# Performance work log

Hardware: AMD Instinct MI355X
Metric: run time of the kernel (lower is better)

The kernel has to match this reference:

```python
import jax, jax.numpy as jnp
import numpy as np

REG = 0.1  # sinkhorn_reg from __init__


def setup_inputs() -> dict:
    key = jax.random.key(0)
    ks = jax.random.split(key, 13)
    B, T, C, H, W = 16, 128, 256, 32, 32  # batch, num_tokens, hidden c, mask HxW
    HW = H * W
    s = 0.02
    return {
        "F_a": jax.random.normal(ks[0], (B, T, C), jnp.float32),
        "F_s": jax.random.normal(ks[1], (B, HW, C), jnp.float32),
        "M_s": jax.random.randint(ks[2], (B, H, W), 0, 2, jnp.int32),
        # learned params (torch Linear: y = x @ W + b, W stored here as [in, out])
        "W_aQ": jax.random.normal(ks[3], (C, HW), jnp.float32) * s,
        "b_aQ": jnp.zeros((HW,), jnp.float32),
        "W_sK": jax.random.normal(ks[4], (C, HW), jnp.float32) * s,
        "b_sK": jnp.zeros((HW,), jnp.float32),
        "W_sV": jax.random.normal(ks[5], (C, C), jnp.float32) * s,
        "b_sV": jnp.zeros((C,), jnp.float32),
        "W1": jax.random.normal(ks[6], (C, 3 * C), jnp.float32) * s,
        "b1": jnp.zeros((3 * C,), jnp.float32),
        "W2": jax.random.normal(ks[7], (3 * C, C), jnp.float32) * s,
        "b2": jnp.zeros((C,), jnp.float32),
        "max_iter_ot": 100,
    }


def reference(F_a, F_s, M_s, W_aQ, b_aQ, W_sK, b_sK, W_sV, b_sV, W1, b1, W2, b2, max_iter_ot):
    B, T, _ = F_a.shape
    m = M_s.reshape(B, -1).astype(jnp.float32)              # [B, HW] binary fg mask
    neg = jnp.where(m[:, None, :] == 1.0, 0.0, -jnp.inf)    # additive attention mask

    # Attention_Eqn3: S = softmax(Q_a K_s^T / 1 + M)
    Q = F_a @ W_aQ + b_aQ                                   # [B, T, HW]
    K_s = F_s @ W_sK + b_sK                                 # [B, HW, HW]
    QK = jnp.einsum("bth,bkh->btk", Q, K_s)                 # [B, T, HW]
    S = jax.nn.softmax(QK + neg, axis=2)                    # masked cols -> 0

    # Vectorized masked Sinkhorn OT across the batch.
    # Zero target marginal on masked columns is equivalent to POT's sinkhorn
    # on the foreground-only cost matrix (their v stays 0, zeroing those cols).
    cost = 1.0 - S
    Kmat = jnp.exp(-cost / REG)                             # [B, T, HW], strictly > 0
    num_fg = jnp.sum(m, axis=1, keepdims=True)              # [B, 1]
    bvec = m / num_fg                                       # [B, HW] uniform over fg
    avec = jnp.full((B, T), 1.0 / T, jnp.float32)

    u0 = jnp.full((B, T), 1.0 / T, jnp.float32)
    v0 = jnp.zeros_like(bvec)

    def step(carry, _):
        u, _v = carry
        Ktu = jnp.einsum("bth,bt->bh", Kmat, u)
        v = jnp.where(bvec > 0, bvec / Ktu, 0.0)
        Kv = jnp.einsum("bth,bh->bt", Kmat, v)
        u = avec / Kv
        return (u, v), None

    (u, v), _ = jax.lax.scan(step, (u0, v0), None, length=max_iter_ot)
    S_hat = u[:, :, None] * Kmat * v[:, None, :]            # [B, T, HW]

    # Attention_Eqn7: FFN(S_hat @ V_s); dropout is identity in eval mode
    V_s = F_s @ W_sV + b_sV                                 # [B, HW, C]
    out = jnp.einsum("btk,bkc->btc", S_hat, V_s)            # [B, T, C]
    h = jax.nn.relu(out @ W1 + b1)
    return h @ W2 + b2
```

## Files before the change

### kernel.cpp

```cpp
#include <hip/hip_runtime.h>
#include <cstdint>

#define T_DIM 128
#define C_DIM 256
#define HW_DIM 1024
#define B_DIM 16
#define NJR 8
#define PARTC 640
#define CHK 10
#define TOL 2e-6f
#define LDP 72

typedef __bf16 bf16x8 __attribute__((ext_vector_type(8)));
typedef float f32x4 __attribute__((ext_vector_type(4)));

__device__ __forceinline__ float fast_rcp(float x) {
  return __builtin_amdgcn_rcpf(x);
}

__device__ __forceinline__ unsigned short f2bf(float x) {
  unsigned u = __float_as_uint(x);
  u += 0x7fffu + ((u >> 16) & 1u);
  return (unsigned short)(u >> 16);
}
__device__ __forceinline__ float bf2f(unsigned short h) {
  return __uint_as_float((unsigned)h << 16);
}

__global__ __launch_bounds__(256) void prep_kernel(const int* __restrict__ Ms,
                                                   int* __restrict__ nfg,
                                                   int* __restrict__ pos)
{
  const int b = blockIdx.x, tid = threadIdx.x;
  const int4 m4 = *(const int4*)(Ms + b * HW_DIM + tid * 4);
  const int c = m4.x + m4.y + m4.z + m4.w;
  const int lane = tid & 63, w = tid >> 6;
  int pre = c;
  #pragma unroll
  for (int o = 1; o < 64; o <<= 1) { int t = __shfl_up(pre, (unsigned)o); if (lane >= o) pre += t; }
  __shared__ int wtot[4];
  if (lane == 63) wtot[w] = pre;
  __syncthreads();
  int base = 0;
  #pragma unroll
  for (int i = 0; i < 4; i++) if (i < w) base += wtot[i];
  const int excl = base + pre - c;
  if (tid == 0) nfg[b] = wtot[0] + wtot[1] + wtot[2] + wtot[3];
  int p = excl;
  const int mm[4] = {m4.x, m4.y, m4.z, m4.w};
  #pragma unroll
  for (int q = 0; q < 4; q++) {
    pos[b * HW_DIM + tid * 4 + q] = mm[q] ? p : -1;
    p += mm[q];
  }
}

__global__ __launch_bounds__(256) void wvec_kernel(
    const float* __restrict__ W_aQ, const float* __restrict__ b_aQ,
    const float* __restrict__ W_sK, const float* __restrict__ b_sK,
    float* __restrict__ w0, float* __restrict__ wq, float* __restrict__ s0)
{
  const int wid = blockIdx.x * 4 + (threadIdx.x >> 6);
  const int lane = threadIdx.x & 63;
  if (wid > 512) return;
  float acc = 0.f;
  if (wid < 256) {
    #pragma unroll 4
    for (int j = 0; j < 16; j++) { int h = lane + 64 * j; acc = fmaf(b_aQ[h], W_sK[(size_t)wid * 1024 + h], acc); }
  } else if (wid < 512) {
    const int c = wid - 256;
    #pragma unroll 4
    for (int j = 0; j < 16; j++) { int h = lane + 64 * j; acc = fmaf(W_aQ[(size_t)c * 1024 + h], b_sK[h], acc); }
  } else {
    #pragma unroll 4
    for (int j = 0; j < 16; j++) { int h = lane + 64 * j; acc = fmaf(b_aQ[h], b_sK[h], acc); }
  }
  #pragma unroll
  for (int o = 32; o; o >>= 1) acc += __shfl_xor(acc, o);
  if (lane == 0) {
    if (wid < 256) w0[wid] = acc;
    else if (wid < 512) wq[wid - 256] = acc;
    else s0[0] = acc;
  }
}

__global__ __launch_bounds__(256) void qb_kernel(const float* __restrict__ F_a,
    const float* __restrict__ wq, const float* __restrict__ s0, float* __restrict__ qb)
{
  const int r = blockIdx.x * 4 + (threadIdx.x >> 6);
  const int lane = threadIdx.x & 63;
  float acc = 0.f;
  #pragma unroll
  for (int j = 0; j < 4; j++) { int c = lane + 64 * j; acc = fmaf(F_a[(size_t)r * 256 + c], wq[c], acc); }
  #pragma unroll
  for (int o = 32; o; o >>= 1) acc += __shfl_xor(acc, o);
  if (lane == 0) qb[r] = acc + s0[0];
}

__global__ __launch_bounds__(256) void split_kernel(const float* __restrict__ S,
    unsigned short* __restrict__ Dh, unsigned short* __restrict__ Dl, int n8)
{
  const int i = blockIdx.x * 256 + threadIdx.x;
  if (i >= n8) return;
  const float4 x0 = ((const float4*)S)[2 * i];
  const float4 x1 = ((const float4*)S)[2 * i + 1];
  const float xs[8] = {x0.x, x0.y, x0.z, x0.w, x1.x, x1.y, x1.z, x1.w};
  unsigned hs[8], ls[8];
  #pragma unroll
  for (int q = 0; q < 8; q++) {
    const unsigned short h = f2bf(xs[q]);
    hs[q] = h;
    ls[q] = f2bf(xs[q] - bf2f(h));
  }
  uint4 oh, ol;
  oh.x = hs[0] | (hs[1] << 16); oh.y = hs[2] | (hs[3] << 16);
  oh.z = hs[4] | (hs[5] << 16); oh.w = hs[6] | (hs[7] << 16);
  ol.x = ls[0] | (ls[1] << 16); ol.y = ls[2] | (ls[3] << 16);
  ol.z = ls[4] | (ls[5] << 16); ol.w = ls[6] | (ls[7] << 16);
  ((uint4*)Dh)[i] = oh;
  ((uint4*)Dl)[i] = ol;
}

__global__ __launch_bounds__(256) void splitT_kernel(const float* __restrict__ S, int R, int C,
    long long sS, unsigned short* __restrict__ Dh, unsigned short* __restrict__ Dl, long long sD)
{
  __shared__ float t[32][33];
  const int bz = blockIdx.z;
  S += sS * bz;  Dh += sD * bz;  Dl += sD * bz;
  const int c0 = blockIdx.x * 32, r0 = blockIdx.y * 32;
  const int tx = threadIdx.x & 31, ty = threadIdx.x >> 5;
  #pragma unroll
  for (int i = 0; i < 4; i++) t[ty + 8 * i][tx] = S[(size_t)(r0 + ty + 8 * i) * C + c0 + tx];
  __syncthreads();
  #pragma unroll
  for (int i = 0; i < 4; i++) {
    const int c = ty + 8 * i;
    const float x = t[tx][c];
    const unsigned short h = f2bf(x);
    Dh[(size_t)(c0 + c) * R + r0 + tx] = h;
    Dl[(size_t)(c0 + c) * R + r0 + tx] = f2bf(x - bf2f(h));
  }
}

template<int BIAS, bool RELU, int OUTM>
__global__ __launch_bounds__(256) void mgemm_kernel(
    const unsigned short* __restrict__ Ah, const unsigned short* __restrict__ Al, int lda, long long sA,
    const unsigned short* __restrict__ Bh, const unsigned short* __restrict__ Bl, int ldb, long long sB,
    void* __restrict__ C0, void* __restrict__ C1, int ldc, long long sC,
    int K, const float* __restrict__ bias, int sBias, float bscale)
{
  __shared__ __align__(16) unsigned short AsH[64 * LDP];
  __shared__ __align__(16) unsigned short AsL[64 * LDP];
  __shared__ __align__(16) unsigned short BsH[64 * LDP];
  __shared__ __align__(16) unsigned short BsL[64 * LDP];
  const int bz = blockIdx.z;
  Ah += sA * bz;  Al += sA * bz;  Bh += sB * bz;  Bl += sB * bz;
  const int m0 = blockIdx.y * 64, n0 = blockIdx.x * 64;
  const int tid = threadIdx.x;
  const int lr = tid >> 2, lc = (tid & 3) * 16;
  const int w = tid >> 6, lane = tid & 63;
  const int wm = (w >> 1) * 32, wn = (w & 1) * 32;
  const int fr = lane & 15, fk = (lane >> 4) * 8;
  const f32x4 zz = {0.f, 0.f, 0.f, 0.f};
  f32x4 acc[2][2] = {{zz, zz}, {zz, zz}};
  const size_t abase = (size_t)(m0 + lr) * lda + lc;
  const size_t bbase = (size_t)(n0 + lr) * ldb + lc;
  uint4 ah0 = *(const uint4*)(Ah + abase), ah1 = *(const uint4*)(Ah + abase + 8);
  uint4 al0 = *(const uint4*)(Al + abase), al1 = *(const uint4*)(Al + abase + 8);
  uint4 bh0 = *(const uint4*)(Bh + bbase), bh1 = *(const uint4*)(Bh + bbase + 8);
  uint4 bl0 = *(const uint4*)(Bl + bbase), bl1 = *(const uint4*)(Bl + bbase + 8);
  const int NT = K >> 6;
  for (int t = 0; t < NT; ++t) {
    __syncthreads();
    *(uint4*)&AsH[lr * LDP + lc] = ah0;  *(uint4*)&AsH[lr * LDP + lc + 8] = ah1;
    *(uint4*)&AsL[lr * LDP + lc] = al0;  *(uint4*)&AsL[lr * LDP + lc + 8] = al1;
    *(uint4*)&BsH[lr * LDP + lc] = bh0;  *(uint4*)&BsH[lr * LDP + lc + 8] = bh1;
    *(uint4*)&BsL[lr * LDP + lc] = bl0;  *(uint4*)&BsL[lr * LDP + lc + 8] = bl1;
    __syncthreads();
    if (t + 1 < NT) {
      const size_t ka = abase + (size_t)(t + 1) * 64;
      const size_t kb = bbase + (size_t)(t + 1) * 64;
      ah0 = *(const uint4*)(Ah + ka);  ah1 = *(const uint4*)(Ah + ka + 8);
      al0 = *(const uint4*)(Al + ka);  al1 = *(const uint4*)(Al + ka + 8);
      bh0 = *(const uint4*)(Bh + kb);  bh1 = *(const uint4*)(Bh + kb + 8);
      bl0 = *(const uint4*)(Bl + kb);  bl1 = *(const uint4*)(Bl + kb + 8);
    }
    #pragma unroll
    for (int ks = 0; ks < 2; ++ks) {
      const bf16x8 aH0 = *(const bf16x8*)&AsH[(wm + fr) * LDP + ks * 32 + fk];
      const bf16x8 aH1 = *(const bf16x8*)&AsH[(wm + 16 + fr) * LDP + ks * 32 + fk];
      const bf16x8 aL0 = *(const bf16x8*)&AsL[(wm + fr) * LDP + ks * 32 + fk];
      const bf16x8 aL1 = *(const bf16x8*)&AsL[(wm + 16 + fr) * LDP + ks * 32 + fk];
      const bf16x8 bH0 = *(const bf16x8*)&BsH[(wn + fr) * LDP + ks * 32 + fk];
      const bf16x8 bH1 = *(const bf16x8*)&BsH[(wn + 16 + fr) * LDP + ks * 32 + fk];
      const bf16x8 bL0 = *(const bf16x8*)&BsL[(wn + fr) * LDP + ks * 32 + fk];
      const bf16x8 bL1 = *(const bf16x8*)&BsL[(wn + 16 + fr) * LDP + ks * 32 + fk];
      acc[0][0] = __builtin_amdgcn_mfma_f32_16x16x32_bf16(aH0, bH0, acc[0][0], 0, 0, 0);
      acc[0][1] = __builtin_amdgcn_mfma_f32_16x16x32_bf16(aH0, bH1, acc[0][1], 0, 0, 0);
      acc[1][0] = __builtin_amdgcn_mfma_f32_16x16x32_bf16(aH1, bH0, acc[1][0], 0, 0, 0);
      acc[1][1] = __builtin_amdgcn_mfma_f32_16x16x32_bf16(aH1, bH1, acc[1][1], 0, 0, 0);
      acc[0][0] = __builtin_amdgcn_mfma_f32_16x16x32_bf16(aH0, bL0, acc[0][0], 0, 0, 0);
      acc[0][1] = __builtin_amdgcn_mfma_f32_16x16x32_bf16(aH0, bL1, acc[0][1], 0, 0, 0);
      acc[1][0] = __builtin_amdgcn_mfma_f32_16x16x32_bf16(aH1, bL0, acc[1][0], 0, 0, 0);
      acc[1][1] = __builtin_amdgcn_mfma_f32_16x16x32_bf16(aH1, bL1, acc[1][1], 0, 0, 0);
      acc[0][0] = __builtin_amdgcn_mfma_f32_16x16x32_bf16(aL0, bH0, acc[0][0], 0, 0, 0);
      acc[0][1] = __builtin_amdgcn_mfma_f32_16x16x32_bf16(aL0, bH1, acc[0][1], 0, 0, 0);
      acc[1][0] = __builtin_amdgcn_mfma_f32_16x16x32_bf16(aL1, bH0, acc[1][0], 0, 0, 0);
      acc[1][1] = __builtin_amdgcn_mfma_f32_16x16x32_bf16(aL1, bH1, acc[1][1], 0, 0, 0);
    }
  }
  const long long cb = sC * bz;
  #pragma unroll
  for (int fi = 0; fi < 2; ++fi) {
    #pragma unroll
    for (int r = 0; r < 4; ++r) {
      const int m = m0 + wm + fi * 16 + (lane >> 4) * 4 + r;
      float rb = 0.f;
      if (BIAS == 2) rb = bias[(size_t)sBias * bz + m];
      #pragma unroll
      for (int fj = 0; fj < 2; ++fj) {
        const int n = n0 + wn + fj * 16 + fr;
        float val = acc[fi][fj][r];
        if (BIAS == 1) val += bscale * bias[n];
        if (BIAS == 2) val += rb;
        if (RELU) val = fmaxf(val, 0.f);
        if (OUTM == 0) {
          ((float*)C0)[cb + (size_t)m * ldc + n] = val;
        } else {
          const unsigned short h = f2bf(val);
          ((unsigned short*)C0)[cb + (size_t)m * ldc + n] = h;
          ((unsigned short*)C1)[cb + (size_t)m * ldc + n] = f2bf(val - bf2f(h));
        }
      }
    }
  }
}

__global__ __launch_bounds__(256) void softmax_kernel(
    const float* __restrict__ QK, const int* __restrict__ Ms,
    const int* __restrict__ pos, float* __restrict__ Kc)
{
  const int r = blockIdx.x;
  const int b = r >> 7;
  const int tid = threadIdx.x;
  const float4 x = *(const float4*)(QK + (size_t)r * HW_DIM + tid * 4);
  const int4 m4 = *(const int4*)(Ms + b * HW_DIM + tid * 4);
  float mx = -3.0e38f;
  if (m4.x) mx = x.x;
  if (m4.y) mx = fmaxf(mx, x.y);
  if (m4.z) mx = fmaxf(mx, x.z);
  if (m4.w) mx = fmaxf(mx, x.w);
  #pragma unroll
  for (int o = 32; o; o >>= 1) mx = fmaxf(mx, __shfl_xor(mx, o));
  __shared__ float red[4];
  const int lane = tid & 63, w = tid >> 6;
  if (lane == 0) red[w] = mx;
  __syncthreads();
  const float gmax = fmaxf(fmaxf(red[0], red[1]), fmaxf(red[2], red[3]));
  __syncthreads();
  const float e0 = m4.x ? __expf(x.x - gmax) : 0.f;
  const float e1 = m4.y ? __expf(x.y - gmax) : 0.f;
  const float e2 = m4.z ? __expf(x.z - gmax) : 0.f;
  const float e3 = m4.w ? __expf(x.w - gmax) : 0.f;
  float s = e0 + e1 + e2 + e3;
  #pragma unroll
  for (int o = 32; o; o >>= 1) s += __shfl_xor(s, o);
  if (lane == 0) red[w] = s;
  __syncthreads();
  const float inv = 1.0f / (red[0] + red[1] + red[2] + red[3]);
  const int4 p4 = *(const int4*)(pos + b * HW_DIM + tid * 4);
  const float ev[4] = {e0, e1, e2, e3};
  const int pp[4] = {p4.x, p4.y, p4.z, p4.w};
  #pragma unroll
  for (int q = 0; q < 4; q++)
    if (pp[q] >= 0) Kc[(size_t)r * HW_DIM + pp[q]] = __expf(fmaf(10.f, ev[q] * inv, -10.f));
}

__global__ __launch_bounds__(1024, 4) void sinkhorn_kernel(
    const float* __restrict__ Kc, const int* __restrict__ nfg_arr,
    const int* __restrict__ pos, const int* __restrict__ maxIter,
    float* __restrict__ u_out, float* __restrict__ v_out)
{
  const int b = blockIdx.x;
  const int tid = threadIdx.x;
  const int tg = tid >> 6, kg = tid & 63;
  const int nfg = nfg_arr[b];
  const float inv_nfg = 1.0f / (float)nfg;
  const int niter = *maxIter;
  const int njall = (nfg + 63) >> 6;
  __shared__ float part[16][PARTC];
  __shared__ float v_s[HW_DIM];
  __shared__ float u_s[T_DIM];
  __shared__ int conv;
  const float* KB = Kc + (size_t)(b * T_DIM) * HW_DIM;

  if (njall * 64 <= PARTC) {
    const int njr = (njall < NJR) ? njall : NJR;
    float kreg[8][NJR];
    #pragma unroll
    for (int j = 0; j < NJR; j++) {
      #pragma unroll
      for (int i = 0; i < 8; i++) {
        const int col = kg + 64 * j;
        float vle = 0.f;
        if (j < njr && col < nfg) vle = KB[(size_t)(tg * 8 + i) * HW_DIM + col];
        kreg[i][j] = vle;
      }
    }
    if (tid < T_DIM) u_s[tid] = 1.0f / 128.0f;
    if (tid == 0) conv = 1;
    const float bv = (tid < nfg) ? inv_nfg : 0.f;
    float u_prev = 1.0f / 128.0f;
    __syncthreads();

    for (int it = 0; it < niter; ++it) {
      float uu[8];
      #pragma unroll
      for (int i = 0; i < 8; i++) uu[i] = u_s[tg * 8 + i];
      #pragma unroll
      for (int j = 0; j < NJR; j++) {
        if (j < njr) {
          float s = 0.f;
          #pragma unroll
          for (int i = 0; i < 8; i++) s = fmaf(kreg[i][j], uu[i], s);
          part[tg][kg + 64 * j] = s;
        }
      }
      for (int j = NJR; j < njall; ++j) {
        const int col = kg + 64 * j;
        float s = 0.f;
        #pragma unroll
        for (int i = 0; i < 8; i++) {
          const float kk = (col < nfg) ? KB[(size_t)(tg * 8 + i) * HW_DIM + col] : 0.f;
          s = fmaf(kk, uu[i], s);
        }
        part[tg][col] = s;
      }
      __syncthreads();
      if (it != 0 && (it % CHK) == 0) {
        if (conv) break;
      }
      const int checknow = ((it % CHK) == (CHK - 1));
      if (checknow && tid == 0) conv = 1;
      {
        float vv = 0.f;
        if (tid < nfg) {
          float s = 0.f;
          #pragma unroll
          for (int g = 0; g < 16; g++) s += part[g][tid];
          vv = bv * fast_rcp(s);
        }
        v_s[tid] = vv;
      }
      __syncthreads();
      float vload[NJR];
      #pragma unroll
      for (int j = 0; j < NJR; j++) vload[j] = (j < njr) ? v_s[kg + 64 * j] : 0.f;
      float kv[8];
      #pragma unroll
      for (int i = 0; i < 8; i++) {
        float s = 0.f;
        #pragma unroll
        for (int j = 0; j < NJR; j++) s = fmaf(kreg[i][j], vload[j], s);
        kv[i] = s;
      }
      for (int j = NJR; j < njall; ++j) {
        const int col = kg + 64 * j;
        const float vv = v_s[col];
        #pragma unroll
        for (int i = 0; i < 8; i++) {
          const float kk = (col < nfg) ? KB[(size_t)(tg * 8 + i) * HW_DIM + col] : 0.f;
          kv[i] = fmaf(kk, vv, kv[i]);
        }
      }
      float k2[4];
      #pragma unroll
      for (int p = 0; p < 4; p++) {
        const float g = (kg & 1) ? kv[2 * p] : kv[2 * p + 1];
        const float r = __shfl_xor(g, 1);
        k2[p] = ((kg & 1) ? kv[2 * p + 1] : kv[2 * p]) + r;
      }
      float k3[2];
      #pragma unroll
      for (int q = 0; q < 2; q++) {
        const float g = (kg & 2) ? k2[2 * q] : k2[2 * q + 1];
        const float r = __shfl_xor(g, 2);
        k3[q] = ((kg & 2) ? k2[2 * q + 1] : k2[2 * q]) + r;
      }
      float t;
      {
        const float g = (kg & 4) ? k3[0] : k3[1];
        const float r = __shfl_xor(g, 4);
        t = ((kg & 4) ? k3[1] : k3[0]) + r;
      }
      t += __shfl_xor(t, 8);
      t += __shfl_xor(t, 16);
      t += __shfl_xor(t, 32);
      const float u_new = 0.0078125f * fast_rcp(t);
      if (kg < 8) u_s[tg * 8 + kg] = u_new;
      if (checknow) {
        const int ok = (fabsf(u_new - u_prev) <= TOL * fabsf(u_new));
        if (!__all(ok) && kg == 0) conv = 0;
      }
      u_prev = u_new;
    }
    __syncthreads();
    if (tid < T_DIM) u_out[b * T_DIM + tid] = u_s[tid];
    {
      const int p = pos[b * HW_DIM + tid];
      v_out[b * HW_DIM + tid] = (p >= 0) ? v_s[p] : 0.f;
    }
  } else {
    if (tid < T_DIM) u_s[tid] = 1.0f / 128.0f;
    const float bv = (tid < nfg) ? inv_nfg : 0.f;
    __syncthreads();
    for (int it = 0; it < niter; ++it) {
      float vv = 0.f;
      if (tid < nfg) {
        float s = 0.f;
        for (int t = 0; t < T_DIM; t++) s = fmaf(KB[(size_t)t * HW_DIM + tid], u_s[t], s);
        vv = bv * fast_rcp(s);
      }
      v_s[tid] = vv;
      __syncthreads();
      #pragma unroll
      for (int r8 = 0; r8 < 8; r8++) {
        const int r = tg * 8 + r8;
        float s = 0.f;
        for (int j = 0; j < 16; j++) {
          const int col = kg + 64 * j;
          if (col < nfg) s = fmaf(KB[(size_t)r * HW_DIM + col], v_s[col], s);
        }
        #pragma unroll
        for (int o = 32; o; o >>= 1) s += __shfl_xor(s, o);
        if (kg == 0) u_s[r] = 0.0078125f * fast_rcp(s);
      }
      __syncthreads();
    }
    if (tid < T_DIM) u_out[b * T_DIM + tid] = u_s[tid];
    const int p = pos[b * HW_DIM + tid];
    v_out[b * HW_DIM + tid] = (p >= 0) ? v_s[p] : 0.f;
  }
}

__global__ __launch_bounds__(256) void shat_kernel(const float* __restrict__ Kc,
    const int* __restrict__ pos, const float* __restrict__ u, const float* __restrict__ v,
    unsigned short* __restrict__ ShH, unsigned short* __restrict__ ShL)
{
  const int r = blockIdx.x, b = r >> 7, tid = threadIdx.x;
  const float uu = u[r];
  const int4 p4 = *(const int4*)(pos + b * HW_DIM + tid * 4);
  const float4 vv = *(const float4*)(v + (size_t)b * HW_DIM + tid * 4);
  const float* kr = Kc + (size_t)r * HW_DIM;
  const float ov[4] = {
    (p4.x >= 0) ? uu * kr[p4.x] * vv.x : 0.f,
    (p4.y >= 0) ? uu * kr[p4.y] * vv.y : 0.f,
    (p4.z >= 0) ? uu * kr[p4.z] * vv.z : 0.f,
    (p4.w >= 0) ? uu * kr[p4.w] * vv.w : 0.f };
  unsigned hs[4], ls[4];
  #pragma unroll
  for (int q = 0; q < 4; q++) {
    const unsigned short h = f2bf(ov[q]);
    hs[q] = h;  ls[q] = f2bf(ov[q] - bf2f(h));
  }
  uint2 ph, pl;
  ph.x = hs[0] | (hs[1] << 16);  ph.y = hs[2] | (hs[3] << 16);
  pl.x = ls[0] | (ls[1] << 16);  pl.y = ls[2] | (ls[3] << 16);
  *(uint2*)(ShH + (size_t)r * HW_DIM + tid * 4) = ph;
  *(uint2*)(ShL + (size_t)r * HW_DIM + tid * 4) = pl;
}

extern "C" void kernel_launch(void* const* d_in, const int* in_sizes, int n_in,
                              void* d_out, int out_size, void* d_ws, size_t ws_size,
                              hipStream_t stream)
{
  const float* F_a  = (const float*)d_in[0];
  const float* F_s  = (const float*)d_in[1];
  const int*   M_s  = (const int*)  d_in[2];
  const float* W_aQ = (const float*)d_in[3];
  const float* b_aQ = (const float*)d_in[4];
  const float* W_sK = (const float*)d_in[5];
  const float* b_sK = (const float*)d_in[6];
  const float* W_sV = (const float*)d_in[7];
  const float* b_sV = (const float*)d_in[8];
  const float* W1   = (const float*)d_in[9];
  const float* b1   = (const float*)d_in[10];
  const float* W2   = (const float*)d_in[11];
  const float* b2   = (const float*)d_in[12];
  const int* maxIter = (const int*)d_in[13];
  float* out = (float*)d_out;

  float* f = (float*)d_ws;
  float* w0 = f;  f += 256;
  float* wq = f;  f += 256;
  float* s0 = f;  f += 4;
  float* qb = f;  f += 2048;
  float* u  = f;  f += 2048;
  float* v  = f;  f += 16 * 1024;
  int* nfg  = (int*)f;  f += 16;
  int* pos  = (int*)f;  f += 16 * 1024;
  float* QK = f;  f += 2048 * 1024;
  float* Kc = f;  f += 2048 * 1024;
  unsigned short* us = (unsigned short*)f;
  #define ALLOC2(name, n) unsigned short* name##H = us; us += (n); unsigned short* name##L = us; us += (n);
  ALLOC2(F_a_,  2048 * 256)
  ALLOC2(W_sK_, 256 * 1024)
  ALLOC2(W_aQ_, 256 * 1024)
  ALLOC2(F_s_,  16 * 1024 * 256)
  ALLOC2(F_sT_, 16 * 256 * 1024)
  ALLOC2(MmT_,  256 * 256)
  ALLOC2(W_sVT_, 256 * 256)
  ALLOC2(W1T_, 768 * 256)
  ALLOC2(W2T_, 256 * 768)
  ALLOC2(P_,   2048 * 256)
  ALLOC2(Sh_,  2048 * 1024)
  ALLOC2(A2_,  2048 * 256)
  ALLOC2(o1_,  2048 * 256)
  ALLOC2(hh_,  2048 * 768)
  #undef ALLOC2

  prep_kernel<<<16, 256, 0, stream>>>(M_s, nfg, pos);
  wvec_kernel<<<129, 256, 0, stream>>>(W_aQ, b_aQ, W_sK, b_sK, w0, wq, s0);
  qb_kernel<<<512, 256, 0, stream>>>(F_a, wq, s0, qb);

  split_kernel<<<256, 256, 0, stream>>>(F_a, F_a_H, F_a_L, 2048 * 256 / 8);
  split_kernel<<<128, 256, 0, stream>>>(W_sK, W_sK_H, W_sK_L, 256 * 1024 / 8);
  split_kernel<<<128, 256, 0, stream>>>(W_aQ, W_aQ_H, W_aQ_L, 256 * 1024 / 8);
  split_kernel<<<2048, 256, 0, stream>>>(F_s, F_s_H, F_s_L, 16 * 1024 * 256 / 8);
  splitT_kernel<<<dim3(8, 8, 1),  256, 0, stream>>>(W_sV, 256, 256, 0, W_sVT_H, W_sVT_L, 0);
  splitT_kernel<<<dim3(24, 8, 1), 256, 0, stream>>>(W1, 256, 768, 0, W1T_H, W1T_L, 0);
  splitT_kernel<<<dim3(8, 24, 1), 256, 0, stream>>>(W2, 768, 256, 0, W2T_H, W2T_L, 0);
  splitT_kernel<<<dim3(8, 32, 16), 256, 0, stream>>>(F_s, 1024, 256, 1024 * 256, F_sT_H, F_sT_L, 256 * 1024);

  mgemm_kernel<0,false,1><<<dim3(4,4,1),256,0,stream>>>(
      W_sK_H, W_sK_L, 1024, 0, W_aQ_H, W_aQ_L, 1024, 0, MmT_H, MmT_L, 256, 0, 1024, nullptr, 0, 0.f);
  mgemm_kernel<1,false,1><<<dim3(4,32,1),256,0,stream>>>(
      F_a_H, F_a_L, 256, 0, MmT_H, MmT_L, 256, 0, P_H, P_L, 256, 0, 256, w0, 0, 1.0f);
  mgemm_kernel<2,false,0><<<dim3(16,2,16),256,0,stream>>>(
      P_H, P_L, 256, 128*256, F_s_H, F_s_L, 256, 1024*256, QK, nullptr, 1024, 128LL*1024, 256, qb, 128, 0.f);

  softmax_kernel<<<2048, 256, 0, stream>>>(QK, M_s, pos, Kc);
  sinkhorn_kernel<<<16, 1024, 0, stream>>>(Kc, nfg, pos, maxIter, u, v);
  shat_kernel<<<2048, 256, 0, stream>>>(Kc, pos, u, v, Sh_H, Sh_L);

  mgemm_kernel<0,false,1><<<dim3(4,2,16),256,0,stream>>>(
      Sh_H, Sh_L, 1024, 128*1024, F_sT_H, F_sT_L, 1024, 256*1024, A2_H, A2_L, 256, 128LL*256, 1024, nullptr, 0, 0.f);
  mgemm_kernel<1,false,1><<<dim3(4,32,1),256,0,stream>>>(
      A2_H, A2_L, 256, 0, W_sVT_H, W_sVT_L, 256, 0, o1_H, o1_L, 256, 0, 256, b_sV, 0, 0.0078125f);
  mgemm_kernel<1,true,1><<<dim3(12,32,1),256,0,stream>>>(
      o1_H, o1_L, 256, 0, W1T_H, W1T_L, 256, 0, hh_H, hh_L, 768, 0, 256, b1, 0, 1.0f);
  mgemm_kernel<1,false,0><<<dim3(4,32,1),256,0,stream>>>(
      hh_H, hh_L, 768, 0, W2T_H, W2T_L, 768, 0, out, nullptr, 256, 0, 768, b2, 0, 1.0f);
}
```

Before: 250.2 us.

## Fuse fp32-to-bf16 split and transpose into GEMM tile loads; merge setup kernels

Removes the separate split and splitT pre-pass kernels. The GEMMs now load raw fp32 operands and convert them in-register into hi/lo bf16 pairs while writing the shared-memory tile. For operands stored K-major, the transpose happens through scattered shared-memory stores. It also merges the prep and wvec kernels into one launch. This cuts about ten launches and the intermediate global traffic, but it re-converts each operand for every tile that reads it, and the transposed LDS stores may cause bank conflicts.

```diff
diff --git a/kernel.cpp b/kernel.cpp
--- a/kernel.cpp
+++ b/kernel.cpp
@@ -27,60 +27,58 @@
   return __uint_as_float((unsigned)h << 16);
 }
 
-__global__ __launch_bounds__(256) void prep_kernel(const int* __restrict__ Ms,
-                                                   int* __restrict__ nfg,
-                                                   int* __restrict__ pos)
-{
-  const int b = blockIdx.x, tid = threadIdx.x;
-  const int4 m4 = *(const int4*)(Ms + b * HW_DIM + tid * 4);
-  const int c = m4.x + m4.y + m4.z + m4.w;
-  const int lane = tid & 63, w = tid >> 6;
-  int pre = c;
-  #pragma unroll
-  for (int o = 1; o < 64; o <<= 1) { int t = __shfl_up(pre, (unsigned)o); if (lane >= o) pre += t; }
-  __shared__ int wtot[4];
-  if (lane == 63) wtot[w] = pre;
-  __syncthreads();
-  int base = 0;
-  #pragma unroll
-  for (int i = 0; i < 4; i++) if (i < w) base += wtot[i];
-  const int excl = base + pre - c;
-  if (tid == 0) nfg[b] = wtot[0] + wtot[1] + wtot[2] + wtot[3];
-  int p = excl;
-  const int mm[4] = {m4.x, m4.y, m4.z, m4.w};
-  #pragma unroll
-  for (int q = 0; q < 4; q++) {
-    pos[b * HW_DIM + tid * 4 + q] = mm[q] ? p : -1;
-    p += mm[q];
-  }
-}
-
-__global__ __launch_bounds__(256) void wvec_kernel(
+__global__ __launch_bounds__(256) void setup_kernel(const int* __restrict__ Ms,
+    int* __restrict__ nfg, int* __restrict__ pos,
     const float* __restrict__ W_aQ, const float* __restrict__ b_aQ,
     const float* __restrict__ W_sK, const float* __restrict__ b_sK,
     float* __restrict__ w0, float* __restrict__ wq, float* __restrict__ s0)
 {
-  const int wid = blockIdx.x * 4 + (threadIdx.x >> 6);
-  const int lane = threadIdx.x & 63;
-  if (wid > 512) return;
-  float acc = 0.f;
-  if (wid < 256) {
-    #pragma unroll 4
-    for (int j = 0; j < 16; j++) { int h = lane + 64 * j; acc = fmaf(b_aQ[h], W_sK[(size_t)wid * 1024 + h], acc); }
-  } else if (wid < 512) {
-    const int c = wid - 256;
-    #pragma unroll 4
-    for (int j = 0; j < 16; j++) { int h = lane + 64 * j; acc = fmaf(W_aQ[(size_t)c * 1024 + h], b_sK[h], acc); }
+  const int tid = threadIdx.x;
+  const int lane = tid & 63, w = tid >> 6;
+  if (blockIdx.x < 16) {
+    const int b = blockIdx.x;
+    const int4 m4 = *(const int4*)(Ms + b * HW_DIM + tid * 4);
+    const int c = m4.x + m4.y + m4.z + m4.w;
+    int pre = c;
+    #pragma unroll
+    for (int o = 1; o < 64; o <<= 1) { int t = __shfl_up(pre, (unsigned)o); if (lane >= o) pre += t; }
+    __shared__ int wtot[4];
+    if (lane == 63) wtot[w] = pre;
+    __syncthreads();
+    int base = 0;
+    #pragma unroll
+    for (int i = 0; i < 4; i++) if (i < w) base += wtot[i];
+    const int excl = base + pre - c;
+    if (tid == 0) nfg[b] = wtot[0] + wtot[1] + wtot[2] + wtot[3];
+    int p = excl;
+    const int mm[4] = {m4.x, m4.y, m4.z, m4.w};
+    #pragma unroll
+    for (int q = 0; q < 4; q++) {
+      pos[b * HW_DIM + tid * 4 + q] = mm[q] ? p : -1;
+      p += mm[q];
+    }
   } else {
-    #pragma unroll 4
-    for (int j = 0; j < 16; j++) { int h = lane + 64 * j; acc = fmaf(b_aQ[h], b_sK[h], acc); }
-  }
-  #pragma unroll
-  for (int o = 32; o; o >>= 1) acc += __shfl_xor(acc, o);
-  if (lane == 0) {
-    if (wid < 256) w0[wid] = acc;
-    else if (wid < 512) wq[wid - 256] = acc;
-    else s0[0] = acc;
+    const int wid = (blockIdx.x - 16) * 4 + w;
+    if (wid > 512) return;
+    float acc = 0.f;
+    if (wid < 256) {
+      #pragma unroll 4
+      for (int j = 0; j < 16; j++) { int h = lane + 64 * j; acc = fmaf(b_aQ[h], W_sK[(size_t)wid * 1024 + h], acc); }
+    } else if (wid < 512) {
+      const int c = wid - 256;
+      #pragma unroll 4
+      for (int j = 0; j < 16; j++) { int h = lane + 64 * j; acc = fmaf(W_aQ[(size_t)c * 1024 + h], b_sK[h], acc); }
+    } else {
+      #pragma unroll 4
+      for (int j = 0; j < 16; j++) { int h = lane + 64 * j; acc = fmaf(b_aQ[h], b_sK[h], acc); }
+    }
+    #pragma unroll
+    for (int o = 32; o; o >>= 1) acc += __shfl_xor(acc, o);
+    if (lane == 0) {
+      if (wid < 256) w0[wid] = acc;
+      else if (wid < 512) wq[wid - 256] = acc;
+      else s0[0] = acc;
+    }
   }
 }
 
@@ -97,55 +95,66 @@
   if (lane == 0) qb[r] = acc + s0[0];
 }
 
-__global__ __launch_bounds__(256) void split_kernel(const float* __restrict__ S,
-    unsigned short* __restrict__ Dh, unsigned short* __restrict__ Dl, int n8)
-{
-  const int i = blockIdx.x * 256 + threadIdx.x;
-  if (i >= n8) return;
-  const float4 x0 = ((const float4*)S)[2 * i];
-  const float4 x1 = ((const float4*)S)[2 * i + 1];
-  const float xs[8] = {x0.x, x0.y, x0.z, x0.w, x1.x, x1.y, x1.z, x1.w};
-  unsigned hs[8], ls[8];
-  #pragma unroll
-  for (int q = 0; q < 8; q++) {
-    const unsigned short h = f2bf(xs[q]);
-    hs[q] = h;
-    ls[q] = f2bf(xs[q] - bf2f(h));
-  }
-  uint4 oh, ol;
-  oh.x = hs[0] | (hs[1] << 16); oh.y = hs[2] | (hs[3] << 16);
-  oh.z = hs[4] | (hs[5] << 16); oh.w = hs[6] | (hs[7] << 16);
-  ol.x = ls[0] | (ls[1] << 16); ol.y = ls[2] | (ls[3] << 16);
-  ol.z = ls[4] | (ls[5] << 16); ol.w = ls[6] | (ls[7] << 16);
-  ((uint4*)Dh)[i] = oh;
-  ((uint4*)Dl)[i] = ol;
-}
-
-__global__ __launch_bounds__(256) void splitT_kernel(const float* __restrict__ S, int R, int C,
-    long long sS, unsigned short* __restrict__ Dh, unsigned short* __restrict__ Dl, long long sD)
-{
-  __shared__ float t[32][33];
-  const int bz = blockIdx.z;
-  S += sS * bz;  Dh += sD * bz;  Dl += sD * bz;
-  const int c0 = blockIdx.x * 32, r0 = blockIdx.y * 32;
-  const int tx = threadIdx.x & 31, ty = threadIdx.x >> 5;
-  #pragma unroll
-  for (int i = 0; i < 4; i++) t[ty + 8 * i][tx] = S[(size_t)(r0 + ty + 8 * i) * C + c0 + tx];
-  __syncthreads();
-  #pragma unroll
-  for (int i = 0; i < 4; i++) {
-    const int c = ty + 8 * i;
-    const float x = t[tx][c];
-    const unsigned short h = f2bf(x);
-    Dh[(size_t)(c0 + c) * R + r0 + tx] = h;
-    Dl[(size_t)(c0 + c) * R + r0 + tx] = f2bf(x - bf2f(h));
-  }
-}
-
-template<int BIAS, bool RELU, int OUTM>
+template<int MODE>
+__device__ __forceinline__ void ldG(uint4 r[4], const void* pH, const void* pL, size_t off) {
+  if constexpr (MODE == 2) {
+    const unsigned short* h = (const unsigned short*)pH + off;
+    const unsigned short* l = (const unsigned short*)pL + off;
+    r[0] = *(const uint4*)h;       r[1] = *(const uint4*)(h + 8);
+    r[2] = *(const uint4*)l;       r[3] = *(const uint4*)(l + 8);
+  } else {
+    const float* s = (const float*)pH + off;
+    r[0] = *(const uint4*)s;       r[1] = *(const uint4*)(s + 4);
+    r[2] = *(const uint4*)(s + 8); r[3] = *(const uint4*)(s + 12);
+  }
+}
+
+template<int MODE>
+__device__ __forceinline__ void stL(const uint4 r[4], unsigned short* __restrict__ H,
+                                    unsigned short* __restrict__ L, int lr, int lc) {
+  if constexpr (MODE == 2) {
+    *(uint4*)&H[lr * LDP + lc] = r[0];  *(uint4*)&H[lr * LDP + lc + 8] = r[1];
+    *(uint4*)&L[lr * LDP + lc] = r[2];  *(uint4*)&L[lr * LDP + lc + 8] = r[3];
+  } else {
+    float xs[16];
+    #pragma unroll
+    for (int q = 0; q < 4; q++) {
+      xs[4 * q + 0] = __uint_as_float(r[q].x);
+      xs[4 * q + 1] = __uint_as_float(r[q].y);
+      xs[4 * q + 2] = __uint_as_float(r[q].z);
+      xs[4 * q + 3] = __uint_as_float(r[q].w);
+    }
+    if constexpr (MODE == 0) {
+      unsigned hw[8], lw[8];
+      #pragma unroll
+      for (int e = 0; e < 8; e++) {
+        const unsigned short h0 = f2bf(xs[2 * e]), h1 = f2bf(xs[2 * e + 1]);
+        hw[e] = (unsigned)h0 | ((unsigned)h1 << 16);
+        const unsigned short l0 = f2bf(xs[2 * e] - bf2f(h0)), l1 = f2bf(xs[2 * e + 1] - bf2f(h1));
+        lw[e] = (unsigned)l0 | ((unsigned)l1 << 16);
+      }
+      uint4 a, b, c, d;
+      a.x = hw[0]; a.y = hw[1]; a.z = hw[2]; a.w = hw[3];
+      b.x = hw[4]; b.y = hw[5]; b.z = hw[6]; b.w = hw[7];
+      c.x = lw[0]; c.y = lw[1]; c.z = lw[2]; c.w = lw[3];
+      d.x = lw[4]; d.y = lw[5]; d.z = lw[6]; d.w = lw[7];
+      *(uint4*)&H[lr * LDP + lc] = a;  *(uint4*)&H[lr * LDP + lc + 8] = b;
+      *(uint4*)&L[lr * LDP + lc] = c;  *(uint4*)&L[lr * LDP + lc + 8] = d;
+    } else {
+      #pragma unroll
+      for (int e = 0; e < 16; e++) {
+        const unsigned short h = f2bf(xs[e]);
+        H[(lc + e) * LDP + lr] = h;
+        L[(lc + e) * LDP + lr] = f2bf(xs[e] - bf2f(h));
+      }
+    }
+  }
+}
+
+template<int AM, int BM, int BIAS, bool RELU, int OUTM>
 __global__ __launch_bounds__(256) void mgemm_kernel(
-    const unsigned short* __restrict__ Ah, const unsigned short* __restrict__ Al, int lda, long long sA,
-    const unsigned short* __restrict__ Bh, const unsigned short* __restrict__ Bl, int ldb, long long sB,
+    const void* __restrict__ Ah, const void* __restrict__ Al, int lda, long long sA,
+    const void* __restrict__ Bh, const void* __restrict__ Bl, int ldb, long long sB,
     void* __restrict__ C0, void* __restrict__ C1, int ldc, long long sC,
     int K, const float* __restrict__ bias, int sBias, float bscale)
 {
@@ -154,7 +163,11 @@
   __shared__ __align__(16) unsigned short BsH[64 * LDP];
   __shared__ __align__(16) unsigned short BsL[64 * LDP];
   const int bz = blockIdx.z;
-  Ah += sA * bz;  Al += sA * bz;  Bh += sB * bz;  Bl += sB * bz;
+  const void *Ab, *Alb, *Bb, *Blb;
+  if constexpr (AM == 2) { Ab = (const unsigned short*)Ah + sA * bz; Alb = (const unsigned short*)Al + sA * bz; }
+  else                   { Ab = (const float*)Ah + sA * bz;          Alb = nullptr; }
+  if constexpr (BM == 2) { Bb = (const unsigned short*)Bh + sB * bz; Blb = (const unsigned short*)Bl + sB * bz; }
+  else                   { Bb = (const float*)Bh + sB * bz;          Blb = nullptr; }
   const int m0 = blockIdx.y * 64, n0 = blockIdx.x * 64;
   const int tid = threadIdx.x;
   const int lr = tid >> 2, lc = (tid & 3) * 16;
@@ -163,27 +176,22 @@
   const int fr = lane & 15, fk = (lane >> 4) * 8;
   const f32x4 zz = {0.f, 0.f, 0.f, 0.f};
   f32x4 acc[2][2] = {{zz, zz}, {zz, zz}};
-  const size_t abase = (size_t)(m0 + lr) * lda + lc;
-  const size_t bbase = (size_t)(n0 + lr) * ldb + lc;
-  uint4 ah0 = *(const uint4*)(Ah + abase), ah1 = *(const uint4*)(Ah + abase + 8);
-  uint4 al0 = *(const uint4*)(Al + abase), al1 = *(const uint4*)(Al + abase + 8);
-  uint4 bh0 = *(const uint4*)(Bh + bbase), bh1 = *(const uint4*)(Bh + bbase + 8);
-  uint4 bl0 = *(const uint4*)(Bl + bbase), bl1 = *(const uint4*)(Bl + bbase + 8);
+  const size_t abase = (AM == 1) ? ((size_t)lr * lda + m0 + lc) : ((size_t)(m0 + lr) * lda + lc);
+  const size_t bbase = (BM == 1) ? ((size_t)lr * ldb + n0 + lc) : ((size_t)(n0 + lr) * ldb + lc);
+  const size_t astep = (AM == 1) ? (size_t)64 * lda : 64;
+  const size_t bstep = (BM == 1) ? (size_t)64 * ldb : 64;
+  uint4 ra[4], rb[4];
+  ldG<AM>(ra, Ab, Alb, abase);
+  ldG<BM>(rb, Bb, Blb, bbase);
   const int NT = K >> 6;
   for (int t = 0; t < NT; ++t) {
     __syncthreads();
-    *(uint4*)&AsH[lr * LDP + lc] = ah0;  *(uint4*)&AsH[lr * LDP + lc + 8] = ah1;
-    *(uint4*)&AsL[lr * LDP + lc] = al0;  *(uint4*)&AsL[lr * LDP + lc + 8] = al1;
-    *(uint4*)&BsH[lr * LDP + lc] = bh0;  *(uint4*)&BsH[lr * LDP + lc + 8] = bh1;
-    *(uint4*)&BsL[lr * LDP + lc] = bl0;  *(uint4*)&BsL[lr * LDP + lc + 8] = bl1;
+    stL<AM>(ra, AsH, AsL, lr, lc);
+    stL<BM>(rb, BsH, BsL, lr, lc);
     __syncthreads();
     if (t + 1 < NT) {
-      const size_t ka = abase + (size_t)(t + 1) * 64;
-      const size_t kb = bbase + (size_t)(t + 1) * 64;
-      ah0 = *(const uint4*)(Ah + ka);  ah1 = *(const uint4*)(Ah + ka + 8);
-      al0 = *(const uint4*)(Al + ka);  al1 = *(const uint4*)(Al + ka + 8);
-      bh0 = *(const uint4*)(Bh + kb);  bh1 = *(const uint4*)(Bh + kb + 8);
-      bl0 = *(const uint4*)(Bl + kb);  bl1 = *(const uint4*)(Bl + kb + 8);
+      ldG<AM>(ra, Ab, Alb, abase + (size_t)(t + 1) * astep);
+      ldG<BM>(rb, Bb, Blb, bbase + (size_t)(t + 1) * bstep);
     }
     #pragma unroll
     for (int ks = 0; ks < 2; ++ks) {
@@ -215,14 +223,14 @@
     #pragma unroll
     for (int r = 0; r < 4; ++r) {
       const int m = m0 + wm + fi * 16 + (lane >> 4) * 4 + r;
-      float rb = 0.f;
-      if (BIAS == 2) rb = bias[(size_t)sBias * bz + m];
+      float rb2 = 0.f;
+      if (BIAS == 2) rb2 = bias[(size_t)sBias * bz + m];
       #pragma unroll
       for (int fj = 0; fj < 2; ++fj) {
         const int n = n0 + wn + fj * 16 + fr;
         float val = acc[fi][fj][r];
         if (BIAS == 1) val += bscale * bias[n];
-        if (BIAS == 2) val += rb;
+        if (BIAS == 2) val += rb2;
         if (RELU) val = fmaxf(val, 0.f);
         if (OUTM == 0) {
           ((float*)C0)[cb + (size_t)m * ldc + n] = val;
@@ -503,15 +511,7 @@
   float* Kc = f;  f += 2048 * 1024;
   unsigned short* us = (unsigned short*)f;
   #define ALLOC2(name, n) unsigned short* name##H = us; us += (n); unsigned short* name##L = us; us += (n);
-  ALLOC2(F_a_,  2048 * 256)
-  ALLOC2(W_sK_, 256 * 1024)
-  ALLOC2(W_aQ_, 256 * 1024)
-  ALLOC2(F_s_,  16 * 1024 * 256)
-  ALLOC2(F_sT_, 16 * 256 * 1024)
-  ALLOC2(MmT_,  256 * 256)
-  ALLOC2(W_sVT_, 256 * 256)
-  ALLOC2(W1T_, 768 * 256)
-  ALLOC2(W2T_, 256 * 768)
+  ALLOC2(MmT_, 256 * 256)
   ALLOC2(P_,   2048 * 256)
   ALLOC2(Sh_,  2048 * 1024)
   ALLOC2(A2_,  2048 * 256)
@@ -519,36 +519,26 @@
   ALLOC2(hh_,  2048 * 768)
   #undef ALLOC2
 
-  prep_kernel<<<16, 256, 0, stream>>>(M_s, nfg, pos);
-  wvec_kernel<<<129, 256, 0, stream>>>(W_aQ, b_aQ, W_sK, b_sK, w0, wq, s0);
+  setup_kernel<<<145, 256, 0, stream>>>(M_s, nfg, pos, W_aQ, b_aQ, W_sK, b_sK, w0, wq, s0);
   qb_kernel<<<512, 256, 0, stream>>>(F_a, wq, s0, qb);
 
-  split_kernel<<<256, 256, 0, stream>>>(F_a, F_a_H, F_a_L, 2048 * 256 / 8);
-  split_kernel<<<128, 256, 0, stream>>>(W_sK, W_sK_H, W_sK_L, 256 * 1024 / 8);
-  split_kernel<<<128, 256, 0, stream>>>(W_aQ, W_aQ_H, W_aQ_L, 256 * 1024 / 8);
-  split_kernel<<<2048, 256, 0, stream>>>(F_s, F_s_H, F_s_L, 16 * 1024 * 256 / 8);
-  splitT_kernel<<<dim3(8, 8, 1),  256, 0, stream>>>(W_sV, 256, 256, 0, W_sVT_H, W_sVT_L, 0);
-  splitT_kernel<<<dim3(24, 8, 1), 256, 0, stream>>>(W1, 256, 768, 0, W1T_H, W1T_L, 0);
-  splitT_kernel<<<dim3(8, 24, 1), 256, 0, stream>>>(W2, 768, 256, 0, W2T_H, W2T_L, 0);
-  splitT_kernel<<<dim3(8, 32, 16), 256, 0, stream>>>(F_s, 1024, 256, 1024 * 256, F_sT_H, F_sT_L, 256 * 1024);
-
-  mgemm_kernel<0,false,1><<<dim3(4,4,1),256,0,stream>>>(
-      W_sK_H, W_sK_L, 1024, 0, W_aQ_H, W_aQ_L, 1024, 0, MmT_H, MmT_L, 256, 0, 1024, nullptr, 0, 0.f);
-  mgemm_kernel<1,false,1><<<dim3(4,32,1),256,0,stream>>>(
-      F_a_H, F_a_L, 256, 0, MmT_H, MmT_L, 256, 0, P_H, P_L, 256, 0, 256, w0, 0, 1.0f);
-  mgemm_kernel<2,false,0><<<dim3(16,2,16),256,0,stream>>>(
-      P_H, P_L, 256, 128*256, F_s_H, F_s_L, 256, 1024*256, QK, nullptr, 1024, 128LL*1024, 256, qb, 128, 0.f);
+  mgemm_kernel<0,0,0,false,1><<<dim3(4,4,1),256,0,stream>>>(
+      W_sK, nullptr, 1024, 0, W_aQ, nullptr, 1024, 0, MmT_H, MmT_L, 256, 0, 1024, nullptr, 0, 0.f);
+  mgemm_kernel<0,2,1,false,1><<<dim3(4,32,1),256,0,stream>>>(
+      F_a, nullptr, 256, 0, MmT_H, MmT_L, 256, 0, P_H, P_L, 256, 0, 256, w0, 0, 1.0f);
+  mgemm_kernel<2,0,2,false,0><<<dim3(16,2,16),256,0,stream>>>(
+      P_H, P_L, 256, 128*256, F_s, nullptr, 256, 1024*256, QK, nullptr, 1024, 128LL*1024, 256, qb, 128, 0.f);
 
   softmax_kernel<<<2048, 256, 0, stream>>>(QK, M_s, pos, Kc);
   sinkhorn_kernel<<<16, 1024, 0, stream>>>(Kc, nfg, pos, maxIter, u, v);
   shat_kernel<<<2048, 256, 0, stream>>>(Kc, pos, u, v, Sh_H, Sh_L);
 
-  mgemm_kernel<0,false,1><<<dim3(4,2,16),256,0,stream>>>(
-      Sh_H, Sh_L, 1024, 128*1024, F_sT_H, F_sT_L, 1024, 256*1024, A2_H, A2_L, 256, 128LL*256, 1024, nullptr, 0, 0.f);
-  mgemm_kernel<1,false,1><<<dim3(4,32,1),256,0,stream>>>(
-      A2_H, A2_L, 256, 0, W_sVT_H, W_sVT_L, 256, 0, o1_H, o1_L, 256, 0, 256, b_sV, 0, 0.0078125f);
-  mgemm_kernel<1,true,1><<<dim3(12,32,1),256,0,stream>>>(
-      o1_H, o1_L, 256, 0, W1T_H, W1T_L, 256, 0, hh_H, hh_L, 768, 0, 256, b1, 0, 1.0f);
-  mgemm_kernel<1,false,0><<<dim3(4,32,1),256,0,stream>>>(
-      hh_H, hh_L, 768, 0, W2T_H, W2T_L, 768, 0, out, nullptr, 256, 0, 768, b2, 0, 1.0f);
-}
+  mgemm_kernel<2,1,0,false,1><<<dim3(4,2,16),256,0,stream>>>(
+      Sh_H, Sh_L, 1024, 128*1024, F_s, nullptr, 256, 1024*256, A2_H, A2_L, 256, 128LL*256, 1024, nullptr, 0, 0.f);
+  mgemm_kernel<2,1,1,false,1><<<dim3(4,32,1),256,0,stream>>>(
+      A2_H, A2_L, 256, 0, W_sV, nullptr, 256, 0, o1_H, o1_L, 256, 0, 256, b_sV, 0, 0.0078125f);
+  mgemm_kernel<2,1,1,true,1><<<dim3(12,32,1),256,0,stream>>>(
+      o1_H, o1_L, 256, 0, W1, nullptr, 768, 0, hh_H, hh_L, 768, 0, 256, b1, 0, 1.0f);
+  mgemm_kernel<2,1,1,false,0><<<dim3(4,32,1),256,0,stream>>>(
+      hh_H, hh_L, 768, 0, W2, nullptr, 256, 0, out, nullptr, 256, 0, 768, b2, 0, 1.0f);
+}
```

New measurement: 271.0 us. 1.08x slower.
